# Optimization experiments

Hardware: AMD Instinct MI355X
Metric: run time of the kernel (lower is better)

## Reference

```python
import jax, jax.numpy as jnp
import numpy as np

N_DRUG = 572
D = 512
K = 64          # neighbor_sample_size
T = 30000       # tail entities
R = 200         # relations
MAX_DEG = 32    # padded invariant_adj neighbor count
EPS = 1e-5


def setup_inputs() -> dict:
    key = jax.random.key(0)
    ks = jax.random.split(key, 10)
    return {
        "drug_embed_W": jax.random.normal(ks[0], (N_DRUG, D), jnp.float32),
        "rela_embed_W": jax.random.normal(ks[1], (R, D), jnp.float32),
        "ent_embed_W": jax.random.normal(ks[2], (T, D), jnp.float32),
        "Wa": jax.random.normal(ks[3], (D, D), jnp.float32) / np.float32(np.sqrt(D)),
        "lin_W": jax.random.normal(ks[4], (2 * D, D), jnp.float32) / np.float32(np.sqrt(2 * D)),
        "lin_b": jnp.zeros((D,), jnp.float32),
        "gamma": jnp.ones((D,), jnp.float32),
        "beta": jnp.zeros((D,), jnp.float32),
        "drug_name": jnp.arange(N_DRUG, dtype=jnp.int64 if jax.config.jax_enable_x64 else jnp.int32),
        "adj_tail": jax.random.randint(ks[5], (N_DRUG, K), 0, T),
        "adj_relation": jax.random.randint(ks[6], (N_DRUG, K), 0, R),
        "nbr_idx": jax.random.randint(ks[7], (N_DRUG, MAX_DEG), 0, N_DRUG),
        "nbr_deg": jax.random.randint(ks[8], (N_DRUG,), 0, MAX_DEG),
        "epoch": 2,
    }


def _forward(drug_embed_W, rela_embed_W, ent_embed_W, Wa, lin_W, lin_b, gamma, beta,
             drug_name, adj_tail, adj_relation, nbr_idx, nbr_deg, epoch):
    drug_e = drug_embed_W[drug_name]          # [N, D]
    rela = rela_embed_W[adj_relation]         # [N, K, D]
    ent = ent_embed_W[adj_tail]               # [N, K, D]

    # relation-aware attention over sampled neighbors (AttentionLayer)
    q = drug_e @ Wa                           # [N, D]
    scores = jnp.einsum('nd,nkd->nk', q, rela) * (1.0 / np.float32(np.sqrt(D)))
    attn = jax.nn.softmax(scores, axis=1)     # [N, K]
    agg = jnp.einsum('nk,nkd->nd', attn, ent) # [N, D]

    # Linear1: Linear(2D->D) + ReLU + BatchNorm1d (training-mode batch stats)
    h = jnp.concatenate([agg, drug_e], axis=1) @ lin_W + lin_b
    h = jax.nn.relu(h)
    mean = jnp.mean(h, axis=0)
    var = jnp.var(h, axis=0)                  # biased, as torch BN normalization
    drug_f = (h - mean) * jax.lax.rsqrt(var + EPS) * gamma + beta

    if epoch > 1:
        # sequential per-node neighbor-mean smoothing (in-place semantics)
        mask = (jnp.arange(MAX_DEG)[None, :] < nbr_deg[:, None])  # [N, MAX_DEG]

        def step(f, i):
            pos = nbr_idx[i]
            m = mask[i][:, None].astype(f.dtype)
            s = jnp.sum(f[pos] * m, axis=0)
            deg = nbr_deg[i]
            avg = s / jnp.maximum(deg, 1).astype(f.dtype)
            new = jnp.where(deg > 0, (avg + f[i]) * 0.5, f[i])
            return f.at[i].set(new), None

        drug_f, _ = jax.lax.scan(step, drug_f, jnp.arange(N_DRUG))
    return drug_f


def reference(drug_embed_W, rela_embed_W, ent_embed_W, Wa, lin_W, lin_b, gamma, beta,
              drug_name, adj_tail, adj_relation, nbr_idx, nbr_deg, epoch):
    return _forward(drug_embed_W, rela_embed_W, ent_embed_W, Wa, lin_W, lin_b, gamma, beta,
                    drug_name, adj_tail, adj_relation, nbr_idx, nbr_deg, epoch)
```

## Files before the change

kernel.cpp:

```cpp
#include <hip/hip_runtime.h>

#define N_DRUG 572
#define DIM 512
#define MAXDEG 32
#define FS 17

__global__ __launch_bounds__(256) void prep_kernel(
    const float* __restrict__ Wa, const float* __restrict__ relaW,
    const float* __restrict__ linW, float* __restrict__ linP,
    float* __restrict__ relaP)
{
    const int b = blockIdx.x;
    const int t = threadIdx.x;
    if (b < 512) {
        const int g = b * 256 + t;
        const int c = g & 511, k4 = g >> 9;
        const float4 v = make_float4(linW[(size_t)(k4 * 4 + 0) * 512 + c],
                                     linW[(size_t)(k4 * 4 + 1) * 512 + c],
                                     linW[(size_t)(k4 * 4 + 2) * 512 + c],
                                     linW[(size_t)(k4 * 4 + 3) * 512 + c]);
        *(float4*)&linP[((size_t)(c >> 6) * 256 + k4) * 256 + (c & 63) * 4] = v;
        return;
    }
    const int bb = b - 512;
    const int rb = bb >> 5, kb = bb & 31;
    const int wv = t >> 6, l = t & 63;
    const int r0 = rb * 16 + wv * 4;
    const int k0 = kb * 16;

    float a[4][8];
    #pragma unroll
    for (int rr = 0; rr < 4; ++rr) {
        const float4* ap = (const float4*)(relaW + (size_t)min(r0 + rr, 199) * 512 + l * 8);
        const float4 x = ap[0], y = ap[1];
        a[rr][0] = x.x; a[rr][1] = x.y; a[rr][2] = x.z; a[rr][3] = x.w;
        a[rr][4] = y.x; a[rr][5] = y.y; a[rr][6] = y.z; a[rr][7] = y.w;
    }
    float acc[64];
    #pragma unroll
    for (int i = 0; i < 64; ++i) acc[i] = 0.f;
    #pragma unroll
    for (int kk = 0; kk < 16; ++kk) {
        const float4* bp = (const float4*)(Wa + (size_t)(k0 + kk) * 512 + l * 8);
        const float4 x = bp[0], y = bp[1];
        const float bv[8] = {x.x, x.y, x.z, x.w, y.x, y.y, y.z, y.w};
        #pragma unroll
        for (int rr = 0; rr < 4; ++rr) {
            float s = acc[rr * 16 + kk];
            #pragma unroll
            for (int j = 0; j < 8; ++j) s = fmaf(a[rr][j], bv[j], s);
            acc[rr * 16 + kk] = s;
        }
    }
    #pragma unroll
    for (int off = 1; off <= 32; off <<= 1) {
        #pragma unroll
        for (int i = 0; i < 64; ++i) acc[i] += __shfl_xor(acc[i], off, 64);
    }
    float outv = acc[0];
    #pragma unroll
    for (int i = 1; i < 64; ++i) outv = (l == i) ? acc[i] : outv;
    const int rr = l >> 4, kk = l & 15;
    if (r0 + rr < 200) relaP[(size_t)(r0 + rr) * 512 + k0 + kk] = outv;
}

__global__ __launch_bounds__(256) void attn_kernel(
    const float* __restrict__ drugW, const float* __restrict__ relaP,
    const float* __restrict__ entW, const int* __restrict__ dn,
    const int* __restrict__ adj_tail, const int* __restrict__ adj_rel,
    float* __restrict__ cat)
{
    __shared__ float at[64];
    __shared__ int tails[64];
    __shared__ int rels[64];
    const int d = blockIdx.x;
    const int t = threadIdx.x;
    const int w = t >> 6, lane = t & 63;

    if (t < 64) {
        tails[t] = adj_tail[d * 64 + t];
        rels[t]  = adj_rel[d * 64 + t];
    }
    const int rd = dn[d];
    float qv[8];
    {
        const float4* qp = (const float4*)(drugW + (size_t)rd * 512 + lane * 8);
        const float4 x = qp[0], y = qp[1];
        qv[0] = x.x; qv[1] = x.y; qv[2] = x.z; qv[3] = x.w;
        qv[4] = y.x; qv[5] = y.y; qv[6] = y.z; qv[7] = y.w;
    }
    __syncthreads();

    #pragma unroll 4
    for (int kk = 0; kk < 16; ++kk) {
        const int k = w * 16 + kk;
        const float4* p = (const float4*)(relaP + (size_t)rels[k] * 512 + lane * 8);
        const float4 x = p[0], y = p[1];
        float s = 0.f;
        s = fmaf(qv[0], x.x, s); s = fmaf(qv[1], x.y, s);
        s = fmaf(qv[2], x.z, s); s = fmaf(qv[3], x.w, s);
        s = fmaf(qv[4], y.x, s); s = fmaf(qv[5], y.y, s);
        s = fmaf(qv[6], y.z, s); s = fmaf(qv[7], y.w, s);
        #pragma unroll
        for (int off = 32; off >= 1; off >>= 1) s += __shfl_xor(s, off, 64);
        if (lane == 0) at[k] = s * 0.0441941738241592f;
    }
    __syncthreads();

    if (w == 0) {
        const float s = at[lane];
        float m = s;
        #pragma unroll
        for (int off = 32; off >= 1; off >>= 1) m = fmaxf(m, __shfl_xor(m, off, 64));
        const float e = __expf(s - m);
        float sum = e;
        #pragma unroll
        for (int off = 32; off >= 1; off >>= 1) sum += __shfl_xor(sum, off, 64);
        at[lane] = e / sum;
    }
    __syncthreads();

    {
        const int c2 = t * 2;
        float a0 = 0.f, a1 = 0.f;
        #pragma unroll 8
        for (int k = 0; k < 64; ++k) {
            const float ak = at[k];
            const float2 e = *(const float2*)(entW + (size_t)tails[k] * 512 + c2);
            a0 = fmaf(ak, e.x, a0);
            a1 = fmaf(ak, e.y, a1);
        }
        float* o = cat + (size_t)d * 1024;
        *(float2*)&o[c2] = make_float2(a0, a1);
        const float2 de = *(const float2*)(drugW + (size_t)rd * 512 + c2);
        *(float2*)&o[512 + c2] = de;
    }
}

__global__ __launch_bounds__(512) void gemm_h(
    const float* __restrict__ A, const float* __restrict__ linP,
    const float* __restrict__ bias, float* __restrict__ out)
{
    __shared__ float red[8][8][128];
    const int t = threadIdx.x;
    const int wv = t >> 6, lane = t & 63;
    const int r0 = blockIdx.x * 8;
    const int half = lane >> 5;
    const int cw = (lane * 2) & 63;

    const float* wp = linP + ((size_t)(blockIdx.y * 2 + half) * 256 + wv * 32) * 256
                    + cw * 4;
    const float* ap[8];
    #pragma unroll
    for (int r = 0; r < 8; ++r)
        ap[r] = A + (size_t)min(r0 + r, N_DRUG - 1) * 1024 + wv * 128;

    float acc0[8] = {0.f, 0.f, 0.f, 0.f, 0.f, 0.f, 0.f, 0.f};
    float acc1[8] = {0.f, 0.f, 0.f, 0.f, 0.f, 0.f, 0.f, 0.f};
    #pragma unroll 2
    for (int k4 = 0; k4 < 32; ++k4) {
        const float4 w0 = *(const float4*)(wp + (size_t)k4 * 256);
        const float4 w1 = *(const float4*)(wp + (size_t)k4 * 256 + 4);
        #pragma unroll
        for (int r = 0; r < 8; ++r) {
            const float4 a = *(const float4*)(ap[r] + k4 * 4);
            acc0[r] = fmaf(a.x, w0.x, acc0[r]);
            acc0[r] = fmaf(a.y, w0.y, acc0[r]);
            acc0[r] = fmaf(a.z, w0.z, acc0[r]);
            acc0[r] = fmaf(a.w, w0.w, acc0[r]);
            acc1[r] = fmaf(a.x, w1.x, acc1[r]);
            acc1[r] = fmaf(a.y, w1.y, acc1[r]);
            acc1[r] = fmaf(a.z, w1.z, acc1[r]);
            acc1[r] = fmaf(a.w, w1.w, acc1[r]);
        }
    }
    #pragma unroll
    for (int r = 0; r < 8; ++r)
        *(float2*)&red[wv][r][lane * 2] = make_float2(acc0[r], acc1[r]);
    __syncthreads();

    #pragma unroll
    for (int u = 0; u < 2; ++u) {
        const int o = u * 512 + t;
        const int r = o >> 7, cc = o & 127;
        if (r0 + r < N_DRUG) {
            float v = red[0][r][cc];
            #pragma unroll
            for (int w = 1; w < 8; ++w) v += red[w][r][cc];
            v += bias[blockIdx.y * 128 + cc];
            out[(size_t)(r0 + r) * 512 + blockIdx.y * 128 + cc] = fmaxf(v, 0.f);
        }
    }
}

__global__ __launch_bounds__(512) void scan_kernel(
    float* hout, const float* __restrict__ gamma, const float* __restrict__ beta,
    const int* __restrict__ nbr_idx, const int* __restrict__ nbr_deg,
    const int* __restrict__ epoch)
{
    __shared__ float fs[(N_DRUG + 1) * FS];
    __shared__ alignas(16) unsigned short offs[N_DRUG * MAXDEG];
    __shared__ float2 ivw[N_DRUG];
    __shared__ int   mxs[N_DRUG];
    __shared__ float part[2][32][16];
    __shared__ float bnp[2][16];

    const int t  = threadIdx.x;
    const int c  = t & 15;
    const int rr = t >> 4;
    const int c0 = blockIdx.x * 16;

    for (int i = t; i < N_DRUG; i += 512) {
        const int d = nbr_deg[i];
        ivw[i] = (d > 0) ? make_float2(0.5f / (float)d, 0.5f) : make_float2(0.f, 1.f);
        const int4* np = (const int4*)&nbr_idx[i * MAXDEG];
        unsigned* op = (unsigned*)&offs[i * MAXDEG];
        int mx = -1;
        #pragma unroll
        for (int u = 0; u < 8; ++u) {
            int4 qq = np[u];
            const int b = u * 4;
            qq.x = (b + 0 < d) ? qq.x : N_DRUG;
            qq.y = (b + 1 < d) ? qq.y : N_DRUG;
            qq.z = (b + 2 < d) ? qq.z : N_DRUG;
            qq.w = (b + 3 < d) ? qq.w : N_DRUG;
            mx = max(mx, (qq.x < i) ? qq.x : -1);
            mx = max(mx, (qq.y < i) ? qq.y : -1);
            mx = max(mx, (qq.z < i) ? qq.z : -1);
            mx = max(mx, (qq.w < i) ? qq.w : -1);
            op[2 * u]     = (unsigned)(qq.x * FS) | ((unsigned)(qq.y * FS) << 16);
            op[2 * u + 1] = (unsigned)(qq.z * FS) | ((unsigned)(qq.w * FS) << 16);
        }
        mxs[i] = mx;
    }

    {
        float sl = 0.f, ql = 0.f;
        for (int r = rr; r < N_DRUG; r += 32) {
            const float v = hout[(size_t)r * DIM + c0 + c];
            fs[r * FS + c] = v;
            sl += v;
            ql = fmaf(v, v, ql);
        }
        part[0][rr][c] = sl;
        part[1][rr][c] = ql;
    }
    if (t < FS) fs[N_DRUG * FS + t] = 0.f;
    __syncthreads();

    if (t < 16) {
        float s = 0.f, sq = 0.f;
        #pragma unroll
        for (int k = 0; k < 32; ++k) { s += part[0][k][t]; sq += part[1][k][t]; }
        const float mean = s * (1.f / N_DRUG);
        const float var = sq * (1.f / N_DRUG) - mean * mean;
        const float rstd = rsqrtf(var + 1e-5f);
        const float scl = gamma[c0 + t] * rstd;
        bnp[0][t] = scl;
        bnp[1][t] = beta[c0 + t] - mean * scl;
    }
    __syncthreads();

    {
        const float scl = bnp[0][c];
        const float shf = bnp[1][c];
        for (int r = rr; r < N_DRUG; r += 32)
            fs[r * FS + c] = fmaf(fs[r * FS + c], scl, shf);
    }
    __syncthreads();

    if (epoch[0] > 1) {
        const int wv   = t >> 6;
        const int lane = t & 63;
        const int j    = lane >> 2;
        const int hh   = (lane >> 1) & 1;
        const int cl   = (wv << 1) | (lane & 1);

        int gs = 0;
        int ge;
        {
            const int jj = 1 + lane;
            const bool flag = (lane >= 15) || (jj >= N_DRUG) ||
                              (mxs[min(jj, N_DRUG - 1)] >= 0);
            ge = 1 + (int)__builtin_ctzll(__ballot(flag) & 0xFFFFULL);
        }
        uint4 ca, cb;
        {
            const uint4* p = (const uint4*)&offs[j * MAXDEG + hh * 16];
            ca = p[0]; cb = p[1];
        }
        while (gs < N_DRUG) {
            const bool pred = (gs + j) < ge;
            float s0 = 0.f, s1 = 0.f;
#define G2(W) { s0 += fs[(W & 0xffffu) + cl]; s1 += fs[(W >> 16) + cl]; }
            if (pred) { G2(ca.x) G2(ca.y) G2(ca.z) G2(ca.w)
                        G2(cb.x) G2(cb.y) G2(cb.z) G2(cb.w) }
#undef G2
            uint4 na, nb;
            {
                const uint4* p = (const uint4*)&offs[min(ge + j, N_DRUG - 1) * MAXDEG + hh * 16];
                na = p[0]; nb = p[1];
            }
            int genext;
            {
                const int jj = ge + 1 + lane;
                const bool flag = (lane >= 15) || (jj >= N_DRUG) ||
                                  (mxs[min(jj, N_DRUG - 1)] >= ge);
                genext = ge + 1 + (int)__builtin_ctzll(__ballot(flag) & 0xFFFFULL);
            }
            float nv = 0.f;
            if (pred) {
                const float cur = fs[(gs + j) * FS + cl];
                const float2 iw = ivw[gs + j];
                float sh = s0 + s1;
                sh += __shfl_xor(sh, 2, 64);
                nv = fmaf(sh, iw.x, cur * iw.y);
            }
            asm volatile("" ::: "memory");
            if (pred && hh == 0) fs[(gs + j) * FS + cl] = nv;
            asm volatile("" ::: "memory");
            gs = ge;
            ge = genext;
            ca = na; cb = nb;
        }
    }
    __syncthreads();

    for (int r = rr; r < N_DRUG; r += 32)
        hout[(size_t)r * DIM + c0 + c] = fs[r * FS + c];
}

extern "C" void kernel_launch(void* const* d_in, const int* in_sizes, int n_in,
                              void* d_out, int out_size, void* d_ws, size_t ws_size,
                              hipStream_t stream)
{
    const float* drugW = (const float*)d_in[0];
    const float* relaW = (const float*)d_in[1];
    const float* entW  = (const float*)d_in[2];
    const float* Wa    = (const float*)d_in[3];
    const float* linW  = (const float*)d_in[4];
    const float* linb  = (const float*)d_in[5];
    const float* gamma = (const float*)d_in[6];
    const float* beta  = (const float*)d_in[7];
    const int* drug_name = (const int*)d_in[8];
    const int* adj_tail  = (const int*)d_in[9];
    const int* adj_rel   = (const int*)d_in[10];
    const int* nbr_idx   = (const int*)d_in[11];
    const int* nbr_deg   = (const int*)d_in[12];
    const int* epoch     = (const int*)d_in[13];

    float* out = (float*)d_out;

    float* linP  = (float*)d_ws;
    float* relaP = (float*)((char*)d_ws + 2097152);
    float* cat   = (float*)((char*)d_ws + 2506752);

    prep_kernel<<<928, 256, 0, stream>>>(Wa, relaW, linW, linP, relaP);
    attn_kernel<<<N_DRUG, 256, 0, stream>>>(drugW, relaP, entW, drug_name,
                                            adj_tail, adj_rel, cat);
    gemm_h<<<dim3(72, 4), 512, 0, stream>>>(cat, linP, linb, out);
    scan_kernel<<<32, 512, 0, stream>>>(out, gamma, beta, nbr_idx, nbr_deg, epoch);
}
```

Before: 226.4 us.

## Split smoothing scan into single-wave blocks covering two columns each

The scan kernel goes from 32 blocks of 512 threads (8 waves, 16 columns per block) to 256 blocks of one wave, each owning 2 columns, with the shared feature stride cut to 3. Batch-norm statistics are now reduced with wave shuffles instead of shared-memory partials, and all block barriers are removed. The aim is to spread the latency-bound sequential scan over many more compute units and avoid LDS contention between waves. In exchange, each block rebuilds the neighbor offset table with only 64 threads, so that setup takes more iterations per block.

```diff
diff --git a/kernel.cpp b/kernel.cpp
--- a/kernel.cpp
+++ b/kernel.cpp
@@ -3,7 +3,7 @@
 #define N_DRUG 572
 #define DIM 512
 #define MAXDEG 32
-#define FS 17
+#define FS 3
 
 __global__ __launch_bounds__(256) void prep_kernel(
     const float* __restrict__ Wa, const float* __restrict__ relaW,
@@ -193,7 +193,7 @@
     }
 }
 
-__global__ __launch_bounds__(512) void scan_kernel(
+__global__ __launch_bounds__(64) void scan_kernel(
     float* hout, const float* __restrict__ gamma, const float* __restrict__ beta,
     const int* __restrict__ nbr_idx, const int* __restrict__ nbr_deg,
     const int* __restrict__ epoch)
@@ -202,19 +202,17 @@
     __shared__ alignas(16) unsigned short offs[N_DRUG * MAXDEG];
     __shared__ float2 ivw[N_DRUG];
     __shared__ int   mxs[N_DRUG];
-    __shared__ float part[2][32][16];
-    __shared__ float bnp[2][16];
-
-    const int t  = threadIdx.x;
-    const int c  = t & 15;
-    const int rr = t >> 4;
-    const int c0 = blockIdx.x * 16;
-
-    for (int i = t; i < N_DRUG; i += 512) {
+
+    const int lane = threadIdx.x;
+    const int col  = lane & 1;
+    const int rg   = lane >> 1;
+    const int c0   = blockIdx.x * 2;
+
+    for (int i = lane; i < N_DRUG; i += 64) {
         const int d = nbr_deg[i];
         ivw[i] = (d > 0) ? make_float2(0.5f / (float)d, 0.5f) : make_float2(0.f, 1.f);
         const int4* np = (const int4*)&nbr_idx[i * MAXDEG];
-        unsigned* op = (unsigned*)&offs[i * MAXDEG];
+        uint2* op = (uint2*)&offs[i * MAXDEG];
         int mx = -1;
         #pragma unroll
         for (int u = 0; u < 8; ++u) {
@@ -228,53 +226,38 @@
             mx = max(mx, (qq.y < i) ? qq.y : -1);
             mx = max(mx, (qq.z < i) ? qq.z : -1);
             mx = max(mx, (qq.w < i) ? qq.w : -1);
-            op[2 * u]     = (unsigned)(qq.x * FS) | ((unsigned)(qq.y * FS) << 16);
-            op[2 * u + 1] = (unsigned)(qq.z * FS) | ((unsigned)(qq.w * FS) << 16);
+            op[u] = make_uint2((unsigned)(qq.x * FS) | ((unsigned)(qq.y * FS) << 16),
+                               (unsigned)(qq.z * FS) | ((unsigned)(qq.w * FS) << 16));
         }
         mxs[i] = mx;
     }
 
-    {
-        float sl = 0.f, ql = 0.f;
-        for (int r = rr; r < N_DRUG; r += 32) {
-            const float v = hout[(size_t)r * DIM + c0 + c];
-            fs[r * FS + c] = v;
-            sl += v;
-            ql = fmaf(v, v, ql);
-        }
-        part[0][rr][c] = sl;
-        part[1][rr][c] = ql;
-    }
-    if (t < FS) fs[N_DRUG * FS + t] = 0.f;
-    __syncthreads();
-
-    if (t < 16) {
-        float s = 0.f, sq = 0.f;
-        #pragma unroll
-        for (int k = 0; k < 32; ++k) { s += part[0][k][t]; sq += part[1][k][t]; }
-        const float mean = s * (1.f / N_DRUG);
-        const float var = sq * (1.f / N_DRUG) - mean * mean;
-        const float rstd = rsqrtf(var + 1e-5f);
-        const float scl = gamma[c0 + t] * rstd;
-        bnp[0][t] = scl;
-        bnp[1][t] = beta[c0 + t] - mean * scl;
-    }
-    __syncthreads();
-
-    {
-        const float scl = bnp[0][c];
-        const float shf = bnp[1][c];
-        for (int r = rr; r < N_DRUG; r += 32)
-            fs[r * FS + c] = fmaf(fs[r * FS + c], scl, shf);
-    }
-    __syncthreads();
+    float sl = 0.f, ql = 0.f;
+    for (int r = rg; r < N_DRUG; r += 32) {
+        const float v = hout[(size_t)r * DIM + c0 + col];
+        fs[r * FS + col] = v;
+        sl += v;
+        ql = fmaf(v, v, ql);
+    }
+    if (lane < FS) fs[N_DRUG * FS + lane] = 0.f;
+    #pragma unroll
+    for (int off = 2; off <= 32; off <<= 1) {
+        sl += __shfl_xor(sl, off, 64);
+        ql += __shfl_xor(ql, off, 64);
+    }
+    const float mean = sl * (1.f / N_DRUG);
+    const float var  = ql * (1.f / N_DRUG) - mean * mean;
+    const float rstd = rsqrtf(var + 1e-5f);
+    const float scl  = gamma[c0 + col] * rstd;
+    const float shf  = beta[c0 + col] - mean * scl;
+
+    for (int r = rg; r < N_DRUG; r += 32)
+        fs[r * FS + col] = fmaf(fs[r * FS + col], scl, shf);
 
     if (epoch[0] > 1) {
-        const int wv   = t >> 6;
-        const int lane = t & 63;
-        const int j    = lane >> 2;
-        const int hh   = (lane >> 1) & 1;
-        const int cl   = (wv << 1) | (lane & 1);
+        const int j  = lane >> 2;
+        const int hh = (lane >> 1) & 1;
+        const int cl = lane & 1;
 
         int gs = 0;
         int ge;
@@ -324,10 +307,9 @@
             ca = na; cb = nb;
         }
     }
-    __syncthreads();
-
-    for (int r = rr; r < N_DRUG; r += 32)
-        hout[(size_t)r * DIM + c0 + c] = fs[r * FS + c];
+
+    for (int r = rg; r < N_DRUG; r += 32)
+        hout[(size_t)r * DIM + c0 + col] = fs[r * FS + col];
 }
 
 extern "C" void kernel_launch(void* const* d_in, const int* in_sizes, int n_in,
@@ -359,5 +341,5 @@
     attn_kernel<<<N_DRUG, 256, 0, stream>>>(drugW, relaP, entW, drug_name,
                                             adj_tail, adj_rel, cat);
     gemm_h<<<dim3(72, 4), 512, 0, stream>>>(cat, linP, linb, out);
-    scan_kernel<<<32, 512, 0, stream>>>(out, gamma, beta, nbr_idx, nbr_deg, epoch);
-}
+    scan_kernel<<<256, 64, 0, stream>>>(out, gamma, beta, nbr_idx, nbr_deg, epoch);
+}
```

Measured after the change: 232.2 us. 2.6% more time.
